# Performance work log

Hardware: AMD Instinct MI355X
Metric: run time of the kernel (lower is better)

The kernel has to match this reference:

```python
import jax, jax.numpy as jnp
import numpy as np

E = 200_000   # edges (messages)
T = 2_000_000 # triplets
N = 20_000    # atoms/nodes
H = 128       # hidden_channels
INT = 64      # int_emb_size
BAS = 8       # basis_emb_size
OUT_EMB = 256 # out_emb_channels
NRAD = 6
SBF_DIM = 7 * 6  # num_spherical * num_radial = 42
NB = 4        # num_blocks
OUTC = 1      # num_targets


def setup_inputs() -> dict:
    key = jax.random.key(0)
    ks = iter(jax.random.split(key, 64))

    def w(shape):
        # glorot-ish scaled weights, stored as [in, out] for x @ W
        return jax.random.normal(next(ks), shape, jnp.float32) / np.sqrt(shape[-2])

    return dict(
        x=jax.random.normal(next(ks), (E, H), jnp.float32),
        rbf=jax.random.normal(next(ks), (E, NRAD), jnp.float32),
        sbf=jax.random.normal(next(ks), (T, SBF_DIM), jnp.float32),
        # interaction block params, stacked over NB blocks
        W_rbf1=w((NB, NRAD, BAS)), W_rbf2=w((NB, BAS, H)),
        W_sbf1=w((NB, SBF_DIM, BAS)), W_sbf2=w((NB, BAS, INT)),
        W_kj=w((NB, H, H)), b_kj=jnp.zeros((NB, H), jnp.float32),
        W_ji=w((NB, H, H)), b_ji=jnp.zeros((NB, H), jnp.float32),
        W_down=w((NB, H, INT)), W_up=w((NB, INT, H)),
        Wb=w((NB, 2, H, H)), bb=jnp.zeros((NB, 2, H), jnp.float32),   # num_before_skip=1 -> 2 linears
        Wa=w((NB, 4, H, H)), ba=jnp.zeros((NB, 4, H), jnp.float32),   # num_after_skip=2 -> 4 linears
        W_lin=w((NB, H, H)), b_lin=jnp.zeros((NB, H), jnp.float32),
        # output block params, stacked over NB+1 blocks
        Wo_rbf=w((NB + 1, NRAD, H)),
        Wo_up=w((NB + 1, H, OUT_EMB)), bo_up=jnp.zeros((NB + 1, OUT_EMB), jnp.float32),
        Wo_lins=w((NB + 1, 3, OUT_EMB, OUT_EMB)), bo_lins=jnp.zeros((NB + 1, 3, OUT_EMB), jnp.float32),
        Wo_out=w((NB + 1, OUT_EMB, OUTC)),
        idx_kj=jax.random.randint(next(ks), (T,), 0, E, jnp.int32),
        idx_ji=jax.random.randint(next(ks), (T,), 0, E, jnp.int32),
        idx_i=jax.random.randint(next(ks), (E,), 0, N, jnp.int32),
        num_nodes=N,
    )


def _interaction(b, x, rbf, sbf, idx_kj, idx_ji, p):
    act = jax.nn.silu
    x_ji = act(x @ p['W_ji'][b] + p['b_ji'][b])
    x_kj = act(x @ p['W_kj'][b] + p['b_kj'][b])
    rbf_t = (rbf @ p['W_rbf1'][b]) @ p['W_rbf2'][b]          # [E,H]
    x_kj = act((x_kj * rbf_t) @ p['W_down'][b])              # [E,INT]
    sbf_t = (sbf @ p['W_sbf1'][b]) @ p['W_sbf2'][b]          # [T,INT]
    m = x_kj[idx_kj] * sbf_t                                  # triplet gather [T,INT]
    agg = jax.ops.segment_sum(m, idx_ji, num_segments=x.shape[0])  # scatter-add [E,INT]
    x_kj = act(agg @ p['W_up'][b])                            # [E,H]
    h = x_ji + x_kj
    # residual layers before skip (1 layer = 2 linears)
    h = h + act(act(h @ p['Wb'][b, 0] + p['bb'][b, 0]) @ p['Wb'][b, 1] + p['bb'][b, 1])
    h = act(h @ p['W_lin'][b] + p['b_lin'][b]) + x
    # residual layers after skip (2 layers = 4 linears)
    for l in range(2):
        h = h + act(act(h @ p['Wa'][b, 2 * l] + p['ba'][b, 2 * l]) @ p['Wa'][b, 2 * l + 1] + p['ba'][b, 2 * l + 1])
    return h


def _output(b, x, rbf, idx_i, num_nodes, p):
    act = jax.nn.silu
    t = (rbf @ p['Wo_rbf'][b]) * x                            # [E,H]
    t = jax.ops.segment_sum(t, idx_i, num_segments=num_nodes) # [N,H]
    t = t @ p['Wo_up'][b] + p['bo_up'][b]
    for l in range(3):
        t = act(t @ p['Wo_lins'][b, l] + p['bo_lins'][b, l])
    return t @ p['Wo_out'][b]                                 # [N,OUTC]


def reference(x, rbf, sbf, W_rbf1, W_rbf2, W_sbf1, W_sbf2, W_kj, b_kj, W_ji, b_ji,
              W_down, W_up, Wb, bb, Wa, ba, W_lin, b_lin,
              Wo_rbf, Wo_up, bo_up, Wo_lins, bo_lins, Wo_out,
              idx_kj, idx_ji, idx_i, num_nodes):
    p = dict(W_rbf1=W_rbf1, W_rbf2=W_rbf2, W_sbf1=W_sbf1, W_sbf2=W_sbf2,
             W_kj=W_kj, b_kj=b_kj, W_ji=W_ji, b_ji=b_ji, W_down=W_down, W_up=W_up,
             Wb=Wb, bb=bb, Wa=Wa, ba=ba, W_lin=W_lin, b_lin=b_lin,
             Wo_rbf=Wo_rbf, Wo_up=Wo_up, bo_up=bo_up,
             Wo_lins=Wo_lins, bo_lins=bo_lins, Wo_out=Wo_out)
    P = _output(0, x, rbf, idx_i, num_nodes, p)
    for b in range(NB):  # fixed small layer loop
        x = _interaction(b, x, rbf, sbf, idx_kj, idx_ji, p)
        P = P + _output(b + 1, x, rbf, idx_i, num_nodes, p)
    return P
```

## Files before the change

kernel.cpp:

```cpp
#include <hip/hip_runtime.h>
#include <hip/hip_bf16.h>

#define E_EDGES 200000
#define T_TRIP  2000000
#define N_NODES 20000
#define H_DIM   128
#define INT_DIM 64
#define BAS     8
#define OUT_EMB 256
#define NRAD    6
#define SBF_D   42
#define NB      4

typedef __attribute__((ext_vector_type(8))) __bf16 bf16x8;
typedef __attribute__((ext_vector_type(4))) float f32x4;
typedef unsigned short u16;

__device__ __forceinline__ float silu_f(float v) { return v / (1.0f + __expf(-v)); }

__device__ __forceinline__ u16 f2bf(float f) {
    unsigned int u = __float_as_uint(f);
    u += 0x7FFF + ((u >> 16) & 1);
    return (u16)(u >> 16);
}
__device__ __forceinline__ float bf2f(u16 h) {
    return __uint_as_float(((unsigned int)h) << 16);
}

__device__ __forceinline__ void st_split4(char* H, char* L, int row, int col0, int stride,
                                          const float v[4]) {
    ushort4 hh, ll;
    u16 h0 = f2bf(v[0]); ll.x = f2bf(v[0] - bf2f(h0)); hh.x = h0;
    u16 h1 = f2bf(v[1]); ll.y = f2bf(v[1] - bf2f(h1)); hh.y = h1;
    u16 h2 = f2bf(v[2]); ll.z = f2bf(v[2] - bf2f(h2)); hh.z = h2;
    u16 h3 = f2bf(v[3]); ll.w = f2bf(v[3] - bf2f(h3)); hh.w = h3;
    int off = (row * stride + col0 * 2) ^ ((row & 7) << 4);
    *reinterpret_cast<ushort4*>(H + off) = hh;
    *reinterpret_cast<ushort4*>(L + off) = ll;
}
__device__ __forceinline__ void ld_split4(const char* H, const char* L, int row, int col0,
                                          int stride, float v[4]) {
    int off = (row * stride + col0 * 2) ^ ((row & 7) << 4);
    ushort4 hh = *reinterpret_cast<const ushort4*>(H + off);
    ushort4 ll = *reinterpret_cast<const ushort4*>(L + off);
    v[0] = bf2f(hh.x) + bf2f(ll.x);
    v[1] = bf2f(hh.y) + bf2f(ll.y);
    v[2] = bf2f(hh.z) + bf2f(ll.z);
    v[3] = bf2f(hh.w) + bf2f(ll.w);
}
__device__ __forceinline__ void st_bf4(char* T, int row, int col0, int stride,
                                       const float v[4]) {
    ushort4 hh;
    hh.x = f2bf(v[0]); hh.y = f2bf(v[1]); hh.z = f2bf(v[2]); hh.w = f2bf(v[3]);
    int off = (row * stride + col0 * 2) ^ ((row & 7) << 4);
    *reinterpret_cast<ushort4*>(T + off) = hh;
}

struct BF8x4 { bf16x8 h[4]; bf16x8 l[4]; };

__device__ __forceinline__ BF8x4 loadB128f(const u16* __restrict__ Bh, const u16* __restrict__ Bl,
                                           int k0, int wn, int l15, int khalf)
{
    BF8x4 f;
    #pragma unroll
    for (int n = 0; n < 4; ++n) {
        size_t bo = (size_t)(wn * 64 + n * 16 + l15) * 128 + k0 + khalf;
        f.h[n] = *reinterpret_cast<const bf16x8*>(Bh + bo);
        f.l[n] = *reinterpret_cast<const bf16x8*>(Bl + bo);
    }
    return f;
}
__device__ __forceinline__ BF8x4 loadB64f(const u16* __restrict__ Bh, const u16* __restrict__ Bl,
                                          int k0, int wn, int l15, int khalf)
{
    BF8x4 f;
    #pragma unroll
    for (int n = 0; n < 4; ++n) {
        size_t bo = (size_t)(wn * 64 + n * 16 + l15) * 64 + k0 + khalf;
        f.h[n] = *reinterpret_cast<const bf16x8*>(Bh + bo);
        f.l[n] = *reinterpret_cast<const bf16x8*>(Bl + bo);
    }
    return f;
}
__device__ __forceinline__ BF8x4 loadB256f(const u16* __restrict__ Bh, const u16* __restrict__ Bl,
                                           int k0, int wn, int l15, int khalf)
{
    BF8x4 f;
    #pragma unroll
    for (int n = 0; n < 4; ++n) {
        size_t bo = (size_t)(wn * 64 + n * 16 + l15) * 256 + k0 + khalf;
        f.h[n] = *reinterpret_cast<const bf16x8*>(Bh + bo);
        f.l[n] = *reinterpret_cast<const bf16x8*>(Bl + bo);
    }
    return f;
}

__device__ __forceinline__ void mfma_cluster(
    const char* AH, const char* AL, int k0, int wm, int l15, int khalf,
    const BF8x4& b, f32x4 acc[2][4])
{
    __builtin_amdgcn_s_setprio(1);
    #pragma unroll
    for (int m = 0; m < 2; ++m) {
        int row = wm * 32 + m * 16 + l15;
        int off = (row * 256 + (k0 + khalf) * 2) ^ ((row & 7) << 4);
        bf16x8 ah = *reinterpret_cast<const bf16x8*>(AH + off);
        bf16x8 al = *reinterpret_cast<const bf16x8*>(AL + off);
        #pragma unroll
        for (int n = 0; n < 4; ++n) {
            acc[m][n] = __builtin_amdgcn_mfma_f32_16x16x32_bf16(b.h[n], ah, acc[m][n], 0, 0, 0);
            acc[m][n] = __builtin_amdgcn_mfma_f32_16x16x32_bf16(b.h[n], al, acc[m][n], 0, 0, 0);
            acc[m][n] = __builtin_amdgcn_mfma_f32_16x16x32_bf16(b.l[n], ah, acc[m][n], 0, 0, 0);
        }
    }
    __builtin_amdgcn_s_setprio(0);
}
__device__ __forceinline__ void mfma_cluster_T(
    const char* T, int k0, int wm, int l15, int khalf,
    const BF8x4& b, f32x4 acc[2][4])
{
    __builtin_amdgcn_s_setprio(1);
    #pragma unroll
    for (int m = 0; m < 2; ++m) {
        int row = wm * 32 + m * 16 + l15;
        int off = (row * 256 + (k0 + khalf) * 2) ^ ((row & 7) << 4);
        bf16x8 a = *reinterpret_cast<const bf16x8*>(T + off);
        #pragma unroll
        for (int n = 0; n < 4; ++n) {
            acc[m][n] = __builtin_amdgcn_mfma_f32_16x16x32_bf16(b.h[n], a, acc[m][n], 0, 0, 0);
            acc[m][n] = __builtin_amdgcn_mfma_f32_16x16x32_bf16(b.l[n], a, acc[m][n], 0, 0, 0);
        }
    }
    __builtin_amdgcn_s_setprio(0);
}
__device__ __forceinline__ void mfma_cluster64(
    const char* AH, const char* AL, int k0, int wm, int l15, int khalf,
    const BF8x4& b, f32x4 acc[2][4])
{
    __builtin_amdgcn_s_setprio(1);
    #pragma unroll
    for (int m = 0; m < 2; ++m) {
        int row = wm * 32 + m * 16 + l15;
        int off = (row * 128 + (k0 + khalf) * 2) ^ ((row & 7) << 4);
        bf16x8 ah = *reinterpret_cast<const bf16x8*>(AH + off);
        bf16x8 al = *reinterpret_cast<const bf16x8*>(AL + off);
        #pragma unroll
        for (int n = 0; n < 4; ++n) {
            acc[m][n] = __builtin_amdgcn_mfma_f32_16x16x32_bf16(b.h[n], ah, acc[m][n], 0, 0, 0);
            acc[m][n] = __builtin_amdgcn_mfma_f32_16x16x32_bf16(b.h[n], al, acc[m][n], 0, 0, 0);
            acc[m][n] = __builtin_amdgcn_mfma_f32_16x16x32_bf16(b.l[n], ah, acc[m][n], 0, 0, 0);
        }
    }
    __builtin_amdgcn_s_setprio(0);
}
__device__ __forceinline__ void mfma_cluster512(
    const char* AH, const char* AL, int k0, int l15, int khalf,
    const BF8x4& b, f32x4 acc[2][4])
{
    __builtin_amdgcn_s_setprio(1);
    #pragma unroll
    for (int m = 0; m < 2; ++m) {
        int row = m * 16 + l15;
        int off = (row * 512 + (k0 + khalf) * 2) ^ ((row & 7) << 4);
        bf16x8 ah = *reinterpret_cast<const bf16x8*>(AH + off);
        bf16x8 al = *reinterpret_cast<const bf16x8*>(AL + off);
        #pragma unroll
        for (int n = 0; n < 4; ++n) {
            acc[m][n] = __builtin_amdgcn_mfma_f32_16x16x32_bf16(b.h[n], ah, acc[m][n], 0, 0, 0);
            acc[m][n] = __builtin_amdgcn_mfma_f32_16x16x32_bf16(b.h[n], al, acc[m][n], 0, 0, 0);
            acc[m][n] = __builtin_amdgcn_mfma_f32_16x16x32_bf16(b.l[n], ah, acc[m][n], 0, 0, 0);
        }
    }
    __builtin_amdgcn_s_setprio(0);
}
__device__ __forceinline__ void mfma_cluster512_T(
    const char* T, int k0, int l15, int khalf,
    const BF8x4& b, f32x4 acc[2][4])
{
    __builtin_amdgcn_s_setprio(1);
    #pragma unroll
    for (int m = 0; m < 2; ++m) {
        int row = m * 16 + l15;
        int off = (row * 512 + (k0 + khalf) * 2) ^ ((row & 7) << 4);
        bf16x8 a = *reinterpret_cast<const bf16x8*>(T + off);
        #pragma unroll
        for (int n = 0; n < 4; ++n) {
            acc[m][n] = __builtin_amdgcn_mfma_f32_16x16x32_bf16(b.h[n], a, acc[m][n], 0, 0, 0);
            acc[m][n] = __builtin_amdgcn_mfma_f32_16x16x32_bf16(b.l[n], a, acc[m][n], 0, 0, 0);
        }
    }
    __builtin_amdgcn_s_setprio(0);
}

__device__ __forceinline__ void mm128_pipe(
    const char* AH, const char* AL,
    const u16* __restrict__ Bh, const u16* __restrict__ Bl, BF8x4& pre,
    const u16* __restrict__ nBh, const u16* __restrict__ nBl,
    int wm, int wn, int l15, int khalf, f32x4 acc[2][4])
{
    BF8x4 c0 = pre;
    BF8x4 c1 = loadB128f(Bh, Bl, 32, wn, l15, khalf);
    mfma_cluster(AH, AL, 0, wm, l15, khalf, c0, acc);
    BF8x4 c2 = loadB128f(Bh, Bl, 64, wn, l15, khalf);
    mfma_cluster(AH, AL, 32, wm, l15, khalf, c1, acc);
    BF8x4 c3 = loadB128f(Bh, Bl, 96, wn, l15, khalf);
    mfma_cluster(AH, AL, 64, wm, l15, khalf, c2, acc);
    if (nBh) pre = loadB128f(nBh, nBl, 0, wn, l15, khalf);
    mfma_cluster(AH, AL, 96, wm, l15, khalf, c3, acc);
}
__device__ __forceinline__ void mm128_pipe_T(
    const char* T,
    const u16* __restrict__ Bh, const u16* __restrict__ Bl, BF8x4& pre,
    const u16* __restrict__ nBh, const u16* __restrict__ nBl,
    int wm, int wn, int l15, int khalf, f32x4 acc[2][4])
{
    BF8x4 c0 = pre;
    BF8x4 c1 = loadB128f(Bh, Bl, 32, wn, l15, khalf);
    mfma_cluster_T(T, 0, wm, l15, khalf, c0, acc);
    BF8x4 c2 = loadB128f(Bh, Bl, 64, wn, l15, khalf);
    mfma_cluster_T(T, 32, wm, l15, khalf, c1, acc);
    BF8x4 c3 = loadB128f(Bh, Bl, 96, wn, l15, khalf);
    mfma_cluster_T(T, 64, wm, l15, khalf, c2, acc);
    if (nBh) pre = loadB128f(nBh, nBl, 0, wn, l15, khalf);
    mfma_cluster_T(T, 96, wm, l15, khalf, c3, acc);
}
__device__ __forceinline__ void mm64_pipe(
    const char* AH, const char* AL,
    const u16* __restrict__ Bh, const u16* __restrict__ Bl, BF8x4& pre,
    const u16* __restrict__ nBh, const u16* __restrict__ nBl,
    int wm, int wn, int l15, int khalf, f32x4 acc[2][4])
{
    BF8x4 c0 = pre;
    BF8x4 c1 = loadB64f(Bh, Bl, 32, wn, l15, khalf);
    mfma_cluster64(AH, AL, 0, wm, l15, khalf, c0, acc);
    if (nBh) pre = loadB128f(nBh, nBl, 0, wn, l15, khalf);
    mfma_cluster64(AH, AL, 32, wm, l15, khalf, c1, acc);
}

__global__ __launch_bounds__(256) void wprep(
    const float* __restrict__ src, u16* __restrict__ hi,
    u16* __restrict__ lo, int K, int N)
{
    int e = blockIdx.x * 256 + threadIdx.x;
    int total = K * N;
    if (e >= total) return;
    size_t base = (size_t)blockIdx.y * total;
    float a = src[base + e];
    int k = e / N, n = e - k * N;
    u16 h = f2bf(a);
    u16 l = f2bf(a - bf2f(h));
    hi[base + (size_t)n * K + k] = h;
    lo[base + (size_t)n * K + k] = l;
}

__global__ __launch_bounds__(256, 2) void pre_fuse(
    const float* __restrict__ X, const float* __restrict__ rbf,
    const float* __restrict__ W1,
    const u16* __restrict__ Wjih, const u16* __restrict__ Wjil, const float* __restrict__ bji,
    const u16* __restrict__ Wkjh, const u16* __restrict__ Wkjl, const float* __restrict__ bkj,
    const float* __restrict__ Wr2,
    const u16* __restrict__ Wdnh, const u16* __restrict__ Wdnl,
    float* __restrict__ E1, float* __restrict__ C1)
{
    __shared__ char smem[49152];
    char* XH = smem;
    char* XL = smem + 16384;
    char* IT = smem + 32768;

    const int tid  = threadIdx.x;
    const int lane = tid & 63;
    const int w    = tid >> 6;
    const int wm   = w >> 1, wn = w & 1;
    const int bm   = blockIdx.x * 64;
    const int l15  = lane & 15;
    const int khalf = (lane >> 4) * 8;
    const int r4   = (lane >> 4) * 4;

    BF8x4 pre = loadB128f(Wjih, Wjil, 0, wn, l15, khalf);

    {
        int r  = tid >> 2;
        int c0 = (tid & 3) * 32;
        const float* p = &X[(size_t)(bm + r) * H_DIM + c0];
        const int swz = (r & 7) << 4;
        #pragma unroll
        for (int q = 0; q < 8; ++q) {
            float4 f = *reinterpret_cast<const float4*>(p + q * 4);
            float vv[4] = {f.x, f.y, f.z, f.w};
            u16 h[4], l[4];
            #pragma unroll
            for (int j = 0; j < 4; ++j) {
                h[j] = f2bf(vv[j]);
                l[j] = f2bf(vv[j] - bf2f(h[j]));
            }
            int off = (r * 256 + c0 * 2 + q * 8) ^ swz;
            *reinterpret_cast<ushort4*>(XH + off) = make_ushort4(h[0], h[1], h[2], h[3]);
            *reinterpret_cast<ushort4*>(XL + off) = make_ushort4(l[0], l[1], l[2], l[3]);
        }
    }
    __syncthreads();

    {
        f32x4 acc[2][4] = {};
        mm128_pipe(XH, XL, Wjih, Wjil, pre, Wkjh, Wkjl, wm, wn, l15, khalf, acc);
        #pragma unroll
        for (int n = 0; n < 4; ++n) {
            int col0 = wn * 64 + n * 16 + r4;
            float4 bv = *reinterpret_cast<const float4*>(&bji[col0]);
            #pragma unroll
            for (int m = 0; m < 2; ++m) {
                int row = wm * 32 + m * 16 + l15;
                float4 o;
                o.x = silu_f(acc[m][n][0] + bv.x);
                o.y = silu_f(acc[m][n][1] + bv.y);
                o.z = silu_f(acc[m][n][2] + bv.z);
                o.w = silu_f(acc[m][n][3] + bv.w);
                *reinterpret_cast<float4*>(&E1[(size_t)(bm + row) * H_DIM + col0]) = o;
            }
        }
    }
    {
        f32x4 acc[2][4] = {};
        mm128_pipe(XH, XL, Wkjh, Wkjl, pre, nullptr, nullptr, wm, wn, l15, khalf, acc);
        float r8v[2][8];
        #pragma unroll
        for (int m = 0; m < 2; ++m) {
            int grow = bm + wm * 32 + m * 16 + l15;
            const float2* rp = reinterpret_cast<const float2*>(&rbf[(size_t)grow * NRAD]);
            float2 q0 = rp[0], q1 = rp[1], q2 = rp[2];
            float rv[NRAD] = {q0.x, q0.y, q1.x, q1.y, q2.x, q2.y};
            #pragma unroll
            for (int j = 0; j < 8; ++j) r8v[m][j] = 0.f;
            #pragma unroll
            for (int k = 0; k < NRAD; ++k)
                #pragma unroll
                for (int j = 0; j < 8; ++j)
                    r8v[m][j] = fmaf(rv[k], W1[k * BAS + j], r8v[m][j]);
        }
        #pragma unroll
        for (int n = 0; n < 4; ++n) {
            int col0 = wn * 64 + n * 16 + r4;
            float4 bvf = *reinterpret_cast<const float4*>(&bkj[col0]);
            float bv[4] = {bvf.x, bvf.y, bvf.z, bvf.w};
            float wrv[8][4];
            #pragma unroll
            for (int j = 0; j < 8; ++j) {
                float4 wf = *reinterpret_cast<const float4*>(&Wr2[j * H_DIM + col0]);
                wrv[j][0] = wf.x; wrv[j][1] = wf.y; wrv[j][2] = wf.z; wrv[j][3] = wf.w;
            }
            #pragma unroll
            for (int m = 0; m < 2; ++m) {
                int row = wm * 32 + m * 16 + l15;
                float v[4];
                #pragma unroll
                for (int r = 0; r < 4; ++r) {
                    float t = silu_f(acc[m][n][r] + bv[r]);
                    float g = 0.f;
                    #pragma unroll
                    for (int j = 0; j < 8; ++j)
                        g = fmaf(r8v[m][j], wrv[j][r], g);
                    v[r] = t * g;
                }
                st_bf4(IT, row, col0, 256, v);
            }
        }
    }
    __syncthreads();

    {
        f32x4 acc[2][2] = {};
        #pragma unroll
        for (int k0 = 0; k0 < 128; k0 += 32) {
            bf16x8 bh[2], bl[2];
            #pragma unroll
            for (int n = 0; n < 2; ++n) {
                size_t bo = (size_t)(wn * 32 + n * 16 + l15) * 128 + k0 + khalf;
                bh[n] = *reinterpret_cast<const bf16x8*>(Wdnh + bo);
                bl[n] = *reinterpret_cast<const bf16x8*>(Wdnl + bo);
            }
            __builtin_amdgcn_s_setprio(1);
            #pragma unroll
            for (int m = 0; m < 2; ++m) {
                int row = wm * 32 + m * 16 + l15;
                int off = (row * 256 + (k0 + khalf) * 2) ^ ((row & 7) << 4);
                bf16x8 a = *reinterpret_cast<const bf16x8*>(IT + off);
                #pragma unroll
                for (int n = 0; n < 2; ++n) {
                    acc[m][n] = __builtin_amdgcn_mfma_f32_16x16x32_bf16(bh[n], a, acc[m][n], 0, 0, 0);
                    acc[m][n] = __builtin_amdgcn_mfma_f32_16x16x32_bf16(bl[n], a, acc[m][n], 0, 0, 0);
                }
            }
            __builtin_amdgcn_s_setprio(0);
        }
        #pragma unroll
        for (int n = 0; n < 2; ++n) {
            int col0 = wn * 32 + n * 16 + r4;
            #pragma unroll
            for (int m = 0; m < 2; ++m) {
                int row = wm * 32 + m * 16 + l15;
                float4 o;
                o.x = silu_f(acc[m][n][0]);
                o.y = silu_f(acc[m][n][1]);
                o.z = silu_f(acc[m][n][2]);
                o.w = silu_f(acc[m][n][3]);
                *reinterpret_cast<float4*>(&C1[(size_t)(bm + row) * INT_DIM + col0]) = o;
            }
        }
    }
}

struct ChainP {
    const u16 *uph, *upl;
    const u16 *b0h, *b0l, *b1h, *b1l;
    const u16 *lnh, *lnl;
    const u16 *a0h, *a0l, *a1h, *a1l, *a2h, *a2l, *a3h, *a3l;
    const float *bb0, *bb1, *blin, *ba0, *ba1, *ba2, *ba3;
};
struct OutP {
    const float* TN;
    const u16 *Uh, *Ul; const float* bu;
    const u16 *L0h, *L0l; const float* b0;
    const u16 *L1h, *L1l; const float* b1;
    const u16 *L2h, *L2l; const float* b2;
    const float* Wo; float* P;
};

__device__ __forceinline__ void post_chain_body(
    char* smem, int bx,
    const float* __restrict__ AGG, const float* __restrict__ E1,
    const float* __restrict__ X, const ChainP& p, float* __restrict__ OUT)
{
    char* SH  = smem;
    char* SL  = smem + 16384;
    char* TMP = smem + 32768;
    char* GH  = TMP;
    char* GL  = TMP + 8192;

    const int tid  = threadIdx.x;
    const int lane = tid & 63;
    const int w    = tid >> 6;
    const int wm   = w >> 1, wn = w & 1;
    const int bm   = bx * 64;
    const int l15  = lane & 15;
    const int khalf = (lane >> 4) * 8;
    const int r4   = (lane >> 4) * 4;

    BF8x4 pre = loadB64f(p.uph, p.upl, 0, wn, l15, khalf);

    {
        int r  = tid >> 2;
        int c0 = (tid & 3) * 16;
        const float* pg = &AGG[(size_t)(bm + r) * INT_DIM + c0];
        const int swz = (r & 7) << 4;
        #pragma unroll
        for (int q = 0; q < 4; ++q) {
            float4 f = *reinterpret_cast<const float4*>(pg + q * 4);
            float vv[4] = {f.x, f.y, f.z, f.w};
            u16 h[4], l[4];
            #pragma unroll
            for (int j = 0; j < 4; ++j) {
                h[j] = f2bf(vv[j]);
                l[j] = f2bf(vv[j] - bf2f(h[j]));
            }
            int off = (r * 128 + c0 * 2 + q * 8) ^ swz;
            *reinterpret_cast<ushort4*>(GH + off) = make_ushort4(h[0], h[1], h[2], h[3]);
            *reinterpret_cast<ushort4*>(GL + off) = make_ushort4(l[0], l[1], l[2], l[3]);
        }
    }
    __syncthreads();

    f32x4 acc[2][4];
    #define ZACC { _Pragma("unroll") for (int m = 0; m < 2; ++m) \
                   _Pragma("unroll") for (int n = 0; n < 4; ++n) \
                       acc[m][n] = f32x4{0.f, 0.f, 0.f, 0.f}; }

    ZACC
    mm64_pipe(GH, GL, p.uph, p.upl, pre, p.b0h, p.b0l, wm, wn, l15, khalf, acc);
    #pragma unroll
    for (int n = 0; n < 4; ++n) {
        int col0 = wn * 64 + n * 16 + r4;
        #pragma unroll
        for (int m = 0; m < 2; ++m) {
            int row = wm * 32 + m * 16 + l15;
            float4 e = *reinterpret_cast<const float4*>(&E1[(size_t)(bm + row) * H_DIM + col0]);
            float v[4];
            v[0] = e.x + silu_f(acc[m][n][0]);
            v[1] = e.y + silu_f(acc[m][n][1]);
            v[2] = e.z + silu_f(acc[m][n][2]);
            v[3] = e.w + silu_f(acc[m][n][3]);
            st_split4(SH, SL, row, col0, 256, v);
        }
    }
    __syncthreads();

    #define STAGE_PLAIN(WH, WL, BIAS, NWH, NWL)                                         \
    {                                                                                   \
        ZACC                                                                            \
        mm128_pipe(SH, SL, WH, WL, pre, NWH, NWL, wm, wn, l15, khalf, acc);             \
        _Pragma("unroll")                                                               \
        for (int n = 0; n < 4; ++n) {                                                   \
            int col0 = wn * 64 + n * 16 + r4;                                           \
            float4 bv = *reinterpret_cast<const float4*>(&BIAS[col0]);                  \
            _Pragma("unroll")                                                           \
            for (int m = 0; m < 2; ++m) {                                               \
                int row = wm * 32 + m * 16 + l15;                                       \
                float v[4];                                                             \
                v[0] = silu_f(acc[m][n][0] + bv.x);                                     \
                v[1] = silu_f(acc[m][n][1] + bv.y);                                     \
                v[2] = silu_f(acc[m][n][2] + bv.z);                                     \
                v[3] = silu_f(acc[m][n][3] + bv.w);                                     \
                st_bf4(TMP, row, col0, 256, v);                                         \
            }                                                                           \
        }                                                                               \
        __syncthreads();                                                                \
    }

    #define STAGE_RES(WH, WL, BIAS, NWH, NWL)                                           \
    {                                                                                   \
        ZACC                                                                            \
        mm128_pipe_T(TMP, WH, WL, pre, NWH, NWL, wm, wn, l15, khalf, acc);              \
        _Pragma("unroll")                                                               \
        for (int n = 0; n < 4; ++n) {                                                   \
            int col0 = wn * 64 + n * 16 + r4;                                           \
            float4 bv = *reinterpret_cast<const float4*>(&BIAS[col0]);                  \
            _Pragma("unroll")                                                           \
            for (int m = 0; m < 2; ++m) {                                               \
                int row = wm * 32 + m * 16 + l15;                                       \
                float v[4];                                                             \
                ld_split4(SH, SL, row, col0, 256, v);                                   \
                v[0] += silu_f(acc[m][n][0] + bv.x);                                    \
                v[1] += silu_f(acc[m][n][1] + bv.y);                                    \
                v[2] += silu_f(acc[m][n][2] + bv.z);                                    \
                v[3] += silu_f(acc[m][n][3] + bv.w);                                    \
                st_split4(SH, SL, row, col0, 256, v);                                   \
            }                                                                           \
        }                                                                               \
        __syncthreads();                                                                \
    }

    STAGE_PLAIN(p.b0h, p.b0l, p.bb0, p.b1h, p.b1l)
    STAGE_RES(p.b1h, p.b1l, p.bb1, p.lnh, p.lnl)

    {
        ZACC
        mm128_pipe(SH, SL, p.lnh, p.lnl, pre, p.a0h, p.a0l, wm, wn, l15, khalf, acc);
        __syncthreads();
        #pragma unroll
        for (int n = 0; n < 4; ++n) {
            int col0 = wn * 64 + n * 16 + r4;
            float4 bv = *reinterpret_cast<const float4*>(&p.blin[col0]);
            #pragma unroll
            for (int m = 0; m < 2; ++m) {
                int row = wm * 32 + m * 16 + l15;
                float4 xv = *reinterpret_cast<const float4*>(&X[(size_t)(bm + row) * H_DIM + col0]);
                float v[4];
                v[0] = silu_f(acc[m][n][0] + bv.x) + xv.x;
                v[1] = silu_f(acc[m][n][1] + bv.y) + xv.y;
                v[2] = silu_f(acc[m][n][2] + bv.z) + xv.z;
                v[3] = silu_f(acc[m][n][3] + bv.w) + xv.w;
                st_split4(SH, SL, row, col0, 256, v);
            }
        }
        __syncthreads();
    }

    STAGE_PLAIN(p.a0h, p.a0l, p.ba0, p.a1h, p.a1l)
    STAGE_RES(p.a1h, p.a1l, p.ba1, p.a2h, p.a2l)
    STAGE_PLAIN(p.a2h, p.a2l, p.ba2, p.a3h, p.a3l)

    {
        ZACC
        mm128_pipe_T(TMP, p.a3h, p.a3l, pre, nullptr, nullptr, wm, wn, l15, khalf, acc);
        #pragma unroll
        for (int n = 0; n < 4; ++n) {
            int col0 = wn * 64 + n * 16 + r4;
            float4 bv = *reinterpret_cast<const float4*>(&p.ba3[col0]);
            #pragma unroll
            for (int m = 0; m < 2; ++m) {
                int row = wm * 32 + m * 16 + l15;
                float v[4];
                ld_split4(SH, SL, row, col0, 256, v);
                float4 o;
                o.x = v[0] + silu_f(acc[m][n][0] + bv.x);
                o.y = v[1] + silu_f(acc[m][n][1] + bv.y);
                o.z = v[2] + silu_f(acc[m][n][2] + bv.z);
                o.w = v[3] + silu_f(acc[m][n][3] + bv.w);
                *reinterpret_cast<float4*>(&OUT[(size_t)(bm + row) * H_DIM + col0]) = o;
            }
        }
    }
    #undef STAGE_PLAIN
    #undef STAGE_RES
    #undef ZACC
}

__device__ __forceinline__ void out_chain_body(char* smem, int bx, const OutP& o)
{
    char* SH  = smem;
    char* SL  = smem + 16384;
    char* TMP = smem + 32768;
    char* XH  = TMP;
    char* XL  = TMP + 8192;

    const int tid  = threadIdx.x;
    const int lane = tid & 63;
    const int wn   = tid >> 6;
    const int bm   = bx * 32;
    const int l15  = lane & 15;
    const int khalf = (lane >> 4) * 8;
    const int r4   = (lane >> 4) * 4;

    {
        int r  = tid >> 3;
        int c0 = (tid & 7) * 16;
        const float* p = &o.TN[(size_t)(bm + r) * H_DIM + c0];
        const int swz = (r & 7) << 4;
        #pragma unroll
        for (int q = 0; q < 4; ++q) {
            float4 f = *reinterpret_cast<const float4*>(p + q * 4);
            float vv[4] = {f.x, f.y, f.z, f.w};
            u16 h[4], l[4];
            #pragma unroll
            for (int j = 0; j < 4; ++j) {
                h[j] = f2bf(vv[j]);
                l[j] = f2bf(vv[j] - bf2f(h[j]));
            }
            int off = (r * 256 + c0 * 2 + q * 8) ^ swz;
            *reinterpret_cast<ushort4*>(XH + off) = make_ushort4(h[0], h[1], h[2], h[3]);
            *reinterpret_cast<ushort4*>(XL + off) = make_ushort4(l[0], l[1], l[2], l[3]);
        }
    }
    __syncthreads();

    f32x4 acc[2][4];
    #define ZACC { _Pragma("unroll") for (int m = 0; m < 2; ++m) \
                   _Pragma("unroll") for (int n = 0; n < 4; ++n) \
                       acc[m][n] = f32x4{0.f, 0.f, 0.f, 0.f}; }

    {
        ZACC
        BF8x4 cur = loadB128f(o.Uh, o.Ul, 0, wn, l15, khalf);
        #pragma unroll
        for (int k = 0; k < 4; ++k) {
            BF8x4 nxt;
            if (k < 3) nxt = loadB128f(o.Uh, o.Ul, 32 * (k + 1), wn, l15, khalf);
            mfma_cluster(XH, XL, 32 * k, 0, l15, khalf, cur, acc);
            if (k < 3) cur = nxt;
        }
        __syncthreads();
        #pragma unroll
        for (int n = 0; n < 4; ++n) {
            int col0 = wn * 64 + n * 16 + r4;
            float4 bv = *reinterpret_cast<const float4*>(&o.bu[col0]);
            #pragma unroll
            for (int m = 0; m < 2; ++m) {
                int row = m * 16 + l15;
                float v[4] = {acc[m][n][0] + bv.x, acc[m][n][1] + bv.y,
                              acc[m][n][2] + bv.z, acc[m][n][3] + bv.w};
                st_split4(SH, SL, row, col0, 512, v);
            }
        }
        __syncthreads();
    }

    {
        ZACC
        BF8x4 cur = loadB256f(o.L0h, o.L0l, 0, wn, l15, khalf);
        #pragma unroll
        for (int k = 0; k < 8; ++k) {
            BF8x4 nxt;
            if (k < 7) nxt = loadB256f(o.L0h, o.L0l, 32 * (k + 1), wn, l15, khalf);
            mfma_cluster512(SH, SL, 32 * k, l15, khalf, cur, acc);
            if (k < 7) cur = nxt;
        }
        #pragma unroll
        for (int n = 0; n < 4; ++n) {
            int col0 = wn * 64 + n * 16 + r4;
            float4 bv = *reinterpret_cast<const float4*>(&o.b0[col0]);
            #pragma unroll
            for (int m = 0; m < 2; ++m) {
                int row = m * 16 + l15;
                float v[4];
                v[0] = silu_f(acc[m][n][0] + bv.x);
                v[1] = silu_f(acc[m][n][1] + bv.y);
                v[2] = silu_f(acc[m][n][2] + bv.z);
                v[3] = silu_f(acc[m][n][3] + bv.w);
                st_bf4(TMP, row, col0, 512, v);
            }
        }
        __syncthreads();
    }

    {
        ZACC
        BF8x4 cur = loadB256f(o.L1h, o.L1l, 0, wn, l15, khalf);
        #pragma unroll
        for (int k = 0; k < 8; ++k) {
            BF8x4 nxt;
            if (k < 7) nxt = loadB256f(o.L1h, o.L1l, 32 * (k + 1), wn, l15, khalf);
            mfma_cluster512_T(TMP, 32 * k, l15, khalf, cur, acc);
            if (k < 7) cur = nxt;
        }
        #pragma unroll
        for (int n = 0; n < 4; ++n) {
            int col0 = wn * 64 + n * 16 + r4;
            float4 bv = *reinterpret_cast<const float4*>(&o.b1[col0]);
            #pragma unroll
            for (int m = 0; m < 2; ++m) {
                int row = m * 16 + l15;
                float v[4];
                v[0] = silu_f(acc[m][n][0] + bv.x);
                v[1] = silu_f(acc[m][n][1] + bv.y);
                v[2] = silu_f(acc[m][n][2] + bv.z);
                v[3] = silu_f(acc[m][n][3] + bv.w);
                st_split4(SH, SL, row, col0, 512, v);
            }
        }
        __syncthreads();
    }

    {
        ZACC
        BF8x4 cur = loadB256f(o.L2h, o.L2l, 0, wn, l15, khalf);
        #pragma unroll
        for (int k = 0; k < 8; ++k) {
            BF8x4 nxt;
            if (k < 7) nxt = loadB256f(o.L2h, o.L2l, 32 * (k + 1), wn, l15, khalf);
            mfma_cluster512(SH, SL, 32 * k, l15, khalf, cur, acc);
            if (k < 7) cur = nxt;
        }
        __syncthreads();
        #pragma unroll
        for (int n = 0; n < 4; ++n) {
            int col0 = wn * 64 + n * 16 + r4;
            float4 bv = *reinterpret_cast<const float4*>(&o.b2[col0]);
            #pragma unroll
            for (int m = 0; m < 2; ++m) {
                int row = m * 16 + l15;
                float v[4];
                v[0] = silu_f(acc[m][n][0] + bv.x);
                v[1] = silu_f(acc[m][n][1] + bv.y);
                v[2] = silu_f(acc[m][n][2] + bv.z);
                v[3] = silu_f(acc[m][n][3] + bv.w);
                st_split4(SH, SL, row, col0, 512, v);
            }
        }
// ... 417 lines not shown
```

Baseline: 4.103 ms.

## Give each wave full-width row strips in edge MLP chains and drop block barriers

```diff
diff --git a/kernel.cpp b/kernel.cpp
--- a/kernel.cpp
+++ b/kernel.cpp
@@ -56,6 +56,79 @@
     *reinterpret_cast<ushort4*>(T + off) = hh;
 }
 
+template<int NT>
+__device__ __forceinline__ void wave_mm128s(
+    const char* AH, const char* AL, int rb,
+    const u16* __restrict__ Bh, const u16* __restrict__ Bl,
+    int l15, int khalf, f32x4 acc[NT])
+{
+    const int row = rb + l15;
+    #pragma unroll
+    for (int k0 = 0; k0 < 128; k0 += 32) {
+        int off = (row * 256 + (k0 + khalf) * 2) ^ ((row & 7) << 4);
+        bf16x8 ah = *reinterpret_cast<const bf16x8*>(AH + off);
+        bf16x8 al = *reinterpret_cast<const bf16x8*>(AL + off);
+        __builtin_amdgcn_s_setprio(1);
+        #pragma unroll
+        for (int n = 0; n < NT; ++n) {
+            size_t bo = (size_t)(n * 16 + l15) * 128 + k0 + khalf;
+            bf16x8 bh = *reinterpret_cast<const bf16x8*>(Bh + bo);
+            bf16x8 bl = *reinterpret_cast<const bf16x8*>(Bl + bo);
+            acc[n] = __builtin_amdgcn_mfma_f32_16x16x32_bf16(bh, ah, acc[n], 0, 0, 0);
+            acc[n] = __builtin_amdgcn_mfma_f32_16x16x32_bf16(bh, al, acc[n], 0, 0, 0);
+            acc[n] = __builtin_amdgcn_mfma_f32_16x16x32_bf16(bl, ah, acc[n], 0, 0, 0);
+        }
+        __builtin_amdgcn_s_setprio(0);
+    }
+}
+template<int NT>
+__device__ __forceinline__ void wave_mm128t(
+    const char* T, int rb,
+    const u16* __restrict__ Bh, const u16* __restrict__ Bl,
+    int l15, int khalf, f32x4 acc[NT])
+{
+    const int row = rb + l15;
+    #pragma unroll
+    for (int k0 = 0; k0 < 128; k0 += 32) {
+        int off = (row * 256 + (k0 + khalf) * 2) ^ ((row & 7) << 4);
+        bf16x8 a = *reinterpret_cast<const bf16x8*>(T + off);
+        __builtin_amdgcn_s_setprio(1);
+        #pragma unroll
+        for (int n = 0; n < NT; ++n) {
+            size_t bo = (size_t)(n * 16 + l15) * 128 + k0 + khalf;
+            bf16x8 bh = *reinterpret_cast<const bf16x8*>(Bh + bo);
+            bf16x8 bl = *reinterpret_cast<const bf16x8*>(Bl + bo);
+            acc[n] = __builtin_amdgcn_mfma_f32_16x16x32_bf16(bh, a, acc[n], 0, 0, 0);
+            acc[n] = __builtin_amdgcn_mfma_f32_16x16x32_bf16(bl, a, acc[n], 0, 0, 0);
+        }
+        __builtin_amdgcn_s_setprio(0);
+    }
+}
+__device__ __forceinline__ void wave_mm64s(
+    const char* AH, const char* AL, int rb,
+    const u16* __restrict__ Bh, const u16* __restrict__ Bl,
+    int l15, int khalf, f32x4 acc[8])
+{
+    const int row = rb + l15;
+    #pragma unroll
+    for (int k0 = 0; k0 < 64; k0 += 32) {
+        int off = (row * 128 + (k0 + khalf) * 2) ^ ((row & 7) << 4);
+        bf16x8 ah = *reinterpret_cast<const bf16x8*>(AH + off);
+        bf16x8 al = *reinterpret_cast<const bf16x8*>(AL + off);
+        __builtin_amdgcn_s_setprio(1);
+        #pragma unroll
+        for (int n = 0; n < 8; ++n) {
+            size_t bo = (size_t)(n * 16 + l15) * 64 + k0 + khalf;
+            bf16x8 bh = *reinterpret_cast<const bf16x8*>(Bh + bo);
+            bf16x8 bl = *reinterpret_cast<const bf16x8*>(Bl + bo);
+            acc[n] = __builtin_amdgcn_mfma_f32_16x16x32_bf16(bh, ah, acc[n], 0, 0, 0);
+            acc[n] = __builtin_amdgcn_mfma_f32_16x16x32_bf16(bh, al, acc[n], 0, 0, 0);
+            acc[n] = __builtin_amdgcn_mfma_f32_16x16x32_bf16(bl, ah, acc[n], 0, 0, 0);
+        }
+        __builtin_amdgcn_s_setprio(0);
+    }
+}
+
 struct BF8x4 { bf16x8 h[4]; bf16x8 l[4]; };
 
 __device__ __forceinline__ BF8x4 loadB128f(const u16* __restrict__ Bh, const u16* __restrict__ Bl,
@@ -70,18 +143,6 @@
     }
     return f;
 }
-__device__ __forceinline__ BF8x4 loadB64f(const u16* __restrict__ Bh, const u16* __restrict__ Bl,
-                                          int k0, int wn, int l15, int khalf)
-{
-    BF8x4 f;
-    #pragma unroll
-    for (int n = 0; n < 4; ++n) {
-        size_t bo = (size_t)(wn * 64 + n * 16 + l15) * 64 + k0 + khalf;
-        f.h[n] = *reinterpret_cast<const bf16x8*>(Bh + bo);
-        f.l[n] = *reinterpret_cast<const bf16x8*>(Bl + bo);
-    }
-    return f;
-}
 __device__ __forceinline__ BF8x4 loadB256f(const u16* __restrict__ Bh, const u16* __restrict__ Bl,
                                            int k0, int wn, int l15, int khalf)
 {
@@ -94,7 +155,6 @@
     }
     return f;
 }
-
 __device__ __forceinline__ void mfma_cluster(
     const char* AH, const char* AL, int k0, int wm, int l15, int khalf,
     const BF8x4& b, f32x4 acc[2][4])
@@ -115,44 +175,6 @@
     }
     __builtin_amdgcn_s_setprio(0);
 }
-__device__ __forceinline__ void mfma_cluster_T(
-    const char* T, int k0, int wm, int l15, int khalf,
-    const BF8x4& b, f32x4 acc[2][4])
-{
-    __builtin_amdgcn_s_setprio(1);
-    #pragma unroll
-    for (int m = 0; m < 2; ++m) {
-        int row = wm * 32 + m * 16 + l15;
-        int off = (row * 256 + (k0 + khalf) * 2) ^ ((row & 7) << 4);
-        bf16x8 a = *reinterpret_cast<const bf16x8*>(T + off);
-        #pragma unroll
-        for (int n = 0; n < 4; ++n) {
-            acc[m][n] = __builtin_amdgcn_mfma_f32_16x16x32_bf16(b.h[n], a, acc[m][n], 0, 0, 0);
-            acc[m][n] = __builtin_amdgcn_mfma_f32_16x16x32_bf16(b.l[n], a, acc[m][n], 0, 0, 0);
-        }
-    }
-    __builtin_amdgcn_s_setprio(0);
-}
-__device__ __forceinline__ void mfma_cluster64(
-    const char* AH, const char* AL, int k0, int wm, int l15, int khalf,
-    const BF8x4& b, f32x4 acc[2][4])
-{
-    __builtin_amdgcn_s_setprio(1);
-    #pragma unroll
-    for (int m = 0; m < 2; ++m) {
-        int row = wm * 32 + m * 16 + l15;
-        int off = (row * 128 + (k0 + khalf) * 2) ^ ((row & 7) << 4);
-        bf16x8 ah = *reinterpret_cast<const bf16x8*>(AH + off);
-        bf16x8 al = *reinterpret_cast<const bf16x8*>(AL + off);
-        #pragma unroll
-        for (int n = 0; n < 4; ++n) {
-            acc[m][n] = __builtin_amdgcn_mfma_f32_16x16x32_bf16(b.h[n], ah, acc[m][n], 0, 0, 0);
-            acc[m][n] = __builtin_amdgcn_mfma_f32_16x16x32_bf16(b.h[n], al, acc[m][n], 0, 0, 0);
-            acc[m][n] = __builtin_amdgcn_mfma_f32_16x16x32_bf16(b.l[n], ah, acc[m][n], 0, 0, 0);
-        }
-    }
-    __builtin_amdgcn_s_setprio(0);
-}
 __device__ __forceinline__ void mfma_cluster512(
     const char* AH, const char* AL, int k0, int l15, int khalf,
     const BF8x4& b, f32x4 acc[2][4])
@@ -190,51 +212,6 @@
         }
     }
     __builtin_amdgcn_s_setprio(0);
-}
-
-__device__ __forceinline__ void mm128_pipe(
-    const char* AH, const char* AL,
-    const u16* __restrict__ Bh, const u16* __restrict__ Bl, BF8x4& pre,
-    const u16* __restrict__ nBh, const u16* __restrict__ nBl,
-    int wm, int wn, int l15, int khalf, f32x4 acc[2][4])
-{
-    BF8x4 c0 = pre;
-    BF8x4 c1 = loadB128f(Bh, Bl, 32, wn, l15, khalf);
-    mfma_cluster(AH, AL, 0, wm, l15, khalf, c0, acc);
-    BF8x4 c2 = loadB128f(Bh, Bl, 64, wn, l15, khalf);
-    mfma_cluster(AH, AL, 32, wm, l15, khalf, c1, acc);
-    BF8x4 c3 = loadB128f(Bh, Bl, 96, wn, l15, khalf);
-    mfma_cluster(AH, AL, 64, wm, l15, khalf, c2, acc);
-    if (nBh) pre = loadB128f(nBh, nBl, 0, wn, l15, khalf);
-    mfma_cluster(AH, AL, 96, wm, l15, khalf, c3, acc);
-}
-__device__ __forceinline__ void mm128_pipe_T(
-    const char* T,
-    const u16* __restrict__ Bh, const u16* __restrict__ Bl, BF8x4& pre,
-    const u16* __restrict__ nBh, const u16* __restrict__ nBl,
-    int wm, int wn, int l15, int khalf, f32x4 acc[2][4])
-{
-    BF8x4 c0 = pre;
-    BF8x4 c1 = loadB128f(Bh, Bl, 32, wn, l15, khalf);
-    mfma_cluster_T(T, 0, wm, l15, khalf, c0, acc);
-    BF8x4 c2 = loadB128f(Bh, Bl, 64, wn, l15, khalf);
-    mfma_cluster_T(T, 32, wm, l15, khalf, c1, acc);
-    BF8x4 c3 = loadB128f(Bh, Bl, 96, wn, l15, khalf);
-    mfma_cluster_T(T, 64, wm, l15, khalf, c2, acc);
-    if (nBh) pre = loadB128f(nBh, nBl, 0, wn, l15, khalf);
-    mfma_cluster_T(T, 96, wm, l15, khalf, c3, acc);
-}
-__device__ __forceinline__ void mm64_pipe(
-    const char* AH, const char* AL,
-    const u16* __restrict__ Bh, const u16* __restrict__ Bl, BF8x4& pre,
-    const u16* __restrict__ nBh, const u16* __restrict__ nBl,
-    int wm, int wn, int l15, int khalf, f32x4 acc[2][4])
-{
-    BF8x4 c0 = pre;
-    BF8x4 c1 = loadB64f(Bh, Bl, 32, wn, l15, khalf);
-    mfma_cluster64(AH, AL, 0, wm, l15, khalf, c0, acc);
-    if (nBh) pre = loadB128f(nBh, nBl, 0, wn, l15, khalf);
-    mfma_cluster64(AH, AL, 32, wm, l15, khalf, c1, acc);
 }
 
 __global__ __launch_bounds__(256) void wprep(
@@ -270,13 +247,12 @@
     const int tid  = threadIdx.x;
     const int lane = tid & 63;
     const int w    = tid >> 6;
-    const int wm   = w >> 1, wn = w & 1;
+    const int rb   = w * 16;
     const int bm   = blockIdx.x * 64;
     const int l15  = lane & 15;
     const int khalf = (lane >> 4) * 8;
     const int r4   = (lane >> 4) * 4;
-
-    BF8x4 pre = loadB128f(Wjih, Wjil, 0, wn, l15, khalf);
+    const int row  = rb + l15;
 
     {
         int r  = tid >> 2;
@@ -298,113 +274,68 @@
             *reinterpret_cast<ushort4*>(XL + off) = make_ushort4(l[0], l[1], l[2], l[3]);
         }
     }
-    __syncthreads();
-
-    {
-        f32x4 acc[2][4] = {};
-        mm128_pipe(XH, XL, Wjih, Wjil, pre, Wkjh, Wkjl, wm, wn, l15, khalf, acc);
-        #pragma unroll
-        for (int n = 0; n < 4; ++n) {
-            int col0 = wn * 64 + n * 16 + r4;
+
+    {
+        f32x4 acc[8] = {};
+        wave_mm128s<8>(XH, XL, rb, Wjih, Wjil, l15, khalf, acc);
+        #pragma unroll
+        for (int n = 0; n < 8; ++n) {
+            int col0 = n * 16 + r4;
             float4 bv = *reinterpret_cast<const float4*>(&bji[col0]);
-            #pragma unroll
-            for (int m = 0; m < 2; ++m) {
-                int row = wm * 32 + m * 16 + l15;
-                float4 o;
-                o.x = silu_f(acc[m][n][0] + bv.x);
-                o.y = silu_f(acc[m][n][1] + bv.y);
-                o.z = silu_f(acc[m][n][2] + bv.z);
-                o.w = silu_f(acc[m][n][3] + bv.w);
-                *reinterpret_cast<float4*>(&E1[(size_t)(bm + row) * H_DIM + col0]) = o;
-            }
-        }
-    }
-    {
-        f32x4 acc[2][4] = {};
-        mm128_pipe(XH, XL, Wkjh, Wkjl, pre, nullptr, nullptr, wm, wn, l15, khalf, acc);
-        float r8v[2][8];
-        #pragma unroll
-        for (int m = 0; m < 2; ++m) {
-            int grow = bm + wm * 32 + m * 16 + l15;
-            const float2* rp = reinterpret_cast<const float2*>(&rbf[(size_t)grow * NRAD]);
+            float4 o;
+            o.x = silu_f(acc[n][0] + bv.x);
+            o.y = silu_f(acc[n][1] + bv.y);
+            o.z = silu_f(acc[n][2] + bv.z);
+            o.w = silu_f(acc[n][3] + bv.w);
+            *reinterpret_cast<float4*>(&E1[(size_t)(bm + row) * H_DIM + col0]) = o;
+        }
+    }
+    {
+        f32x4 acc[8] = {};
+        wave_mm128s<8>(XH, XL, rb, Wkjh, Wkjl, l15, khalf, acc);
+        float r8v[8];
+        {
+            const float2* rp = reinterpret_cast<const float2*>(&rbf[(size_t)(bm + row) * NRAD]);
             float2 q0 = rp[0], q1 = rp[1], q2 = rp[2];
             float rv[NRAD] = {q0.x, q0.y, q1.x, q1.y, q2.x, q2.y};
             #pragma unroll
-            for (int j = 0; j < 8; ++j) r8v[m][j] = 0.f;
+            for (int j = 0; j < 8; ++j) r8v[j] = 0.f;
             #pragma unroll
             for (int k = 0; k < NRAD; ++k)
                 #pragma unroll
                 for (int j = 0; j < 8; ++j)
-                    r8v[m][j] = fmaf(rv[k], W1[k * BAS + j], r8v[m][j]);
-        }
-        #pragma unroll
-        for (int n = 0; n < 4; ++n) {
-            int col0 = wn * 64 + n * 16 + r4;
+                    r8v[j] = fmaf(rv[k], W1[k * BAS + j], r8v[j]);
+        }
+        #pragma unroll
+        for (int n = 0; n < 8; ++n) {
+            int col0 = n * 16 + r4;
             float4 bvf = *reinterpret_cast<const float4*>(&bkj[col0]);
             float bv[4] = {bvf.x, bvf.y, bvf.z, bvf.w};
-            float wrv[8][4];
+            float v[4];
             #pragma unroll
-            for (int j = 0; j < 8; ++j) {
-                float4 wf = *reinterpret_cast<const float4*>(&Wr2[j * H_DIM + col0]);
-                wrv[j][0] = wf.x; wrv[j][1] = wf.y; wrv[j][2] = wf.z; wrv[j][3] = wf.w;
+            for (int r = 0; r < 4; ++r) {
+                float t = silu_f(acc[n][r] + bv[r]);
+                float g = 0.f;
+                #pragma unroll
+                for (int j = 0; j < 8; ++j)
+                    g = fmaf(r8v[j], Wr2[j * H_DIM + col0 + r], g);
+                v[r] = t * g;
             }
-            #pragma unroll
-            for (int m = 0; m < 2; ++m) {
-                int row = wm * 32 + m * 16 + l15;
-                float v[4];
-                #pragma unroll
-                for (int r = 0; r < 4; ++r) {
-                    float t = silu_f(acc[m][n][r] + bv[r]);
-                    float g = 0.f;
-                    #pragma unroll
-                    for (int j = 0; j < 8; ++j)
-                        g = fmaf(r8v[m][j], wrv[j][r], g);
-                    v[r] = t * g;
-                }
-                st_bf4(IT, row, col0, 256, v);
-            }
-        }
-    }
-    __syncthreads();
-
-    {
-        f32x4 acc[2][2] = {};
-        #pragma unroll
-        for (int k0 = 0; k0 < 128; k0 += 32) {
-            bf16x8 bh[2], bl[2];
-            #pragma unroll
-            for (int n = 0; n < 2; ++n) {
-                size_t bo = (size_t)(wn * 32 + n * 16 + l15) * 128 + k0 + khalf;
-                bh[n] = *reinterpret_cast<const bf16x8*>(Wdnh + bo);
-                bl[n] = *reinterpret_cast<const bf16x8*>(Wdnl + bo);
-            }
-            __builtin_amdgcn_s_setprio(1);
-            #pragma unroll
-            for (int m = 0; m < 2; ++m) {
-                int row = wm * 32 + m * 16 + l15;
-                int off = (row * 256 + (k0 + khalf) * 2) ^ ((row & 7) << 4);
-                bf16x8 a = *reinterpret_cast<const bf16x8*>(IT + off);
-                #pragma unroll
-                for (int n = 0; n < 2; ++n) {
-                    acc[m][n] = __builtin_amdgcn_mfma_f32_16x16x32_bf16(bh[n], a, acc[m][n], 0, 0, 0);
-                    acc[m][n] = __builtin_amdgcn_mfma_f32_16x16x32_bf16(bl[n], a, acc[m][n], 0, 0, 0);
-                }
-            }
-            __builtin_amdgcn_s_setprio(0);
-        }
-        #pragma unroll
-        for (int n = 0; n < 2; ++n) {
-            int col0 = wn * 32 + n * 16 + r4;
-            #pragma unroll
-            for (int m = 0; m < 2; ++m) {
-                int row = wm * 32 + m * 16 + l15;
-                float4 o;
-                o.x = silu_f(acc[m][n][0]);
-                o.y = silu_f(acc[m][n][1]);
-                o.z = silu_f(acc[m][n][2]);
-                o.w = silu_f(acc[m][n][3]);
-                *reinterpret_cast<float4*>(&C1[(size_t)(bm + row) * INT_DIM + col0]) = o;
-            }
+            st_bf4(IT, row, col0, 256, v);
+        }
+    }
+    {
+        f32x4 acc[4] = {};
+        wave_mm128t<4>(IT, rb, Wdnh, Wdnl, l15, khalf, acc);
+        #pragma unroll
+        for (int n = 0; n < 4; ++n) {
+            int col0 = n * 16 + r4;
+            float4 o;
+            o.x = silu_f(acc[n][0]);
+            o.y = silu_f(acc[n][1]);
+            o.z = silu_f(acc[n][2]);
+            o.w = silu_f(acc[n][3]);
+            *reinterpret_cast<float4*>(&C1[(size_t)(bm + row) * INT_DIM + col0]) = o;
         }
     }
 }
@@ -439,13 +370,12 @@
     const int tid  = threadIdx.x;
     const int lane = tid & 63;
     const int w    = tid >> 6;
-    const int wm   = w >> 1, wn = w & 1;
+    const int rb   = w * 16;
     const int bm   = bx * 64;
     const int l15  = lane & 15;
     const int khalf = (lane >> 4) * 8;
     const int r4   = (lane >> 4) * 4;
-
-    BF8x4 pre = loadB64f(p.uph, p.upl, 0, wn, l15, khalf);
+    const int row  = rb + l15;
 
     {
         int r  = tid >> 2;
@@ -467,131 +397,104 @@
             *reinterpret_cast<ushort4*>(GL + off) = make_ushort4(l[0], l[1], l[2], l[3]);
         }
     }
-    __syncthreads();
-
-    f32x4 acc[2][4];
-    #define ZACC { _Pragma("unroll") for (int m = 0; m < 2; ++m) \
-                   _Pragma("unroll") for (int n = 0; n < 4; ++n) \
-                       acc[m][n] = f32x4{0.f, 0.f, 0.f, 0.f}; }
-
-    ZACC
-    mm64_pipe(GH, GL, p.uph, p.upl, pre, p.b0h, p.b0l, wm, wn, l15, khalf, acc);
-    #pragma unroll
-    for (int n = 0; n < 4; ++n) {
-        int col0 = wn * 64 + n * 16 + r4;
-        #pragma unroll
-        for (int m = 0; m < 2; ++m) {
-            int row = wm * 32 + m * 16 + l15;
-            float4 e = *reinterpret_cast<const float4*>(&E1[(size_t)(bm + row) * H_DIM + col0]);
+
+    f32x4 acc[8];
+    #define ZACC8 { _Pragma("unroll") for (int n = 0; n < 8; ++n) \
+                        acc[n] = f32x4{0.f, 0.f, 0.f, 0.f}; }
+
+    ZACC8
+    wave_mm64s(GH, GL, rb, p.uph, p.upl, l15, khalf, acc);
+    #pragma unroll
+    for (int n = 0; n < 8; ++n) {
+        int col0 = n * 16 + r4;
+        float4 e = *reinterpret_cast<const float4*>(&E1[(size_t)(bm + row) * H_DIM + col0]);
+        float v[4];
+        v[0] = e.x + silu_f(acc[n][0]);
+        v[1] = e.y + silu_f(acc[n][1]);
+        v[2] = e.z + silu_f(acc[n][2]);
+        v[3] = e.w + silu_f(acc[n][3]);
+        st_split4(SH, SL, row, col0, 256, v);
+    }
+
+    #define STAGE_PLAIN(WH, WL, BIAS)                                                   \
+    {                                                                                   \
+        ZACC8                                                                           \
+        wave_mm128s<8>(SH, SL, rb, WH, WL, l15, khalf, acc);                            \
+        _Pragma("unroll")                                                               \
+        for (int n = 0; n < 8; ++n) {                                                   \
+            int col0 = n * 16 + r4;                                                     \
+            float4 bv = *reinterpret_cast<const float4*>(&BIAS[col0]);                  \
+            float v[4];                                                                 \
+            v[0] = silu_f(acc[n][0] + bv.x);                                            \
+            v[1] = silu_f(acc[n][1] + bv.y);                                            \
+            v[2] = silu_f(acc[n][2] + bv.z);                                            \
+            v[3] = silu_f(acc[n][3] + bv.w);                                            \
+            st_bf4(TMP, row, col0, 256, v);                                             \
+        }                                                                               \
+    }
+
+    #define STAGE_RES(WH, WL, BIAS)                                                     \
+    {                                                                                   \
+        ZACC8                                                                           \
+        wave_mm128t<8>(TMP, rb, WH, WL, l15, khalf, acc);                               \
+        _Pragma("unroll")                                                               \
+        for (int n = 0; n < 8; ++n) {                                                   \
+            int col0 = n * 16 + r4;                                                     \
+            float4 bv = *reinterpret_cast<const float4*>(&BIAS[col0]);                  \
+            float v[4];                                                                 \
+            ld_split4(SH, SL, row, col0, 256, v);                                       \
+            v[0] += silu_f(acc[n][0] + bv.x);                                           \
+            v[1] += silu_f(acc[n][1] + bv.y);                                           \
+            v[2] += silu_f(acc[n][2] + bv.z);                                           \
+            v[3] += silu_f(acc[n][3] + bv.w);                                           \
+            st_split4(SH, SL, row, col0, 256, v);                                       \
+        }                                                                               \
+    }
+
+    STAGE_PLAIN(p.b0h, p.b0l, p.bb0)
+    STAGE_RES(p.b1h, p.b1l, p.bb1)
+
+    {
+        ZACC8
+        wave_mm128s<8>(SH, SL, rb, p.lnh, p.lnl, l15, khalf, acc);
+        #pragma unroll
+        for (int n = 0; n < 8; ++n) {
+            int col0 = n * 16 + r4;
+            float4 bv = *reinterpret_cast<const float4*>(&p.blin[col0]);
+            float4 xv = *reinterpret_cast<const float4*>(&X[(size_t)(bm + row) * H_DIM + col0]);
             float v[4];
-            v[0] = e.x + silu_f(acc[m][n][0]);
-            v[1] = e.y + silu_f(acc[m][n][1]);
-            v[2] = e.z + silu_f(acc[m][n][2]);
-            v[3] = e.w + silu_f(acc[m][n][3]);
+            v[0] = silu_f(acc[n][0] + bv.x) + xv.x;
+            v[1] = silu_f(acc[n][1] + bv.y) + xv.y;
+            v[2] = silu_f(acc[n][2] + bv.z) + xv.z;
+            v[3] = silu_f(acc[n][3] + bv.w) + xv.w;
             st_split4(SH, SL, row, col0, 256, v);
         }
     }
-    __syncthreads();
-
-    #define STAGE_PLAIN(WH, WL, BIAS, NWH, NWL)                                         \
-    {                                                                                   \
-        ZACC                                                                            \
-        mm128_pipe(SH, SL, WH, WL, pre, NWH, NWL, wm, wn, l15, khalf, acc);             \
-        _Pragma("unroll")                                                               \
-        for (int n = 0; n < 4; ++n) {                                                   \
-            int col0 = wn * 64 + n * 16 + r4;                                           \
-            float4 bv = *reinterpret_cast<const float4*>(&BIAS[col0]);                  \
-            _Pragma("unroll")                                                           \
-            for (int m = 0; m < 2; ++m) {                                               \
-                int row = wm * 32 + m * 16 + l15;                                       \
-                float v[4];                                                             \
-                v[0] = silu_f(acc[m][n][0] + bv.x);                                     \
-                v[1] = silu_f(acc[m][n][1] + bv.y);                                     \
-                v[2] = silu_f(acc[m][n][2] + bv.z);                                     \
-                v[3] = silu_f(acc[m][n][3] + bv.w);                                     \
-                st_bf4(TMP, row, col0, 256, v);                                         \
-            }                                                                           \
-        }                                                                               \
-        __syncthreads();                                                                \
-    }
-
-    #define STAGE_RES(WH, WL, BIAS, NWH, NWL)                                           \
-    {                                                                                   \
-        ZACC                                                                            \
-        mm128_pipe_T(TMP, WH, WL, pre, NWH, NWL, wm, wn, l15, khalf, acc);              \
-        _Pragma("unroll")                                                               \
-        for (int n = 0; n < 4; ++n) {                                                   \
-            int col0 = wn * 64 + n * 16 + r4;                                           \
-            float4 bv = *reinterpret_cast<const float4*>(&BIAS[col0]);                  \
-            _Pragma("unroll")                                                           \
-            for (int m = 0; m < 2; ++m) {                                               \
-                int row = wm * 32 + m * 16 + l15;                                       \
-                float v[4];                                                             \
-                ld_split4(SH, SL, row, col0, 256, v);                                   \
-                v[0] += silu_f(acc[m][n][0] + bv.x);                                    \
-                v[1] += silu_f(acc[m][n][1] + bv.y);                                    \
-                v[2] += silu_f(acc[m][n][2] + bv.z);                                    \
-                v[3] += silu_f(acc[m][n][3] + bv.w);                                    \
-                st_split4(SH, SL, row, col0, 256, v);                                   \
-            }                                                                           \
-        }                                                                               \
-        __syncthreads();                                                                \
-    }
-
-    STAGE_PLAIN(p.b0h, p.b0l, p.bb0, p.b1h, p.b1l)
-    STAGE_RES(p.b1h, p.b1l, p.bb1, p.lnh, p.lnl)
-
-    {
-        ZACC
-        mm128_pipe(SH, SL, p.lnh, p.lnl, pre, p.a0h, p.a0l, wm, wn, l15, khalf, acc);
-        __syncthreads();
-        #pragma unroll
-        for (int n = 0; n < 4; ++n) {
-            int col0 = wn * 64 + n * 16 + r4;
-            float4 bv = *reinterpret_cast<const float4*>(&p.blin[col0]);
-            #pragma unroll
-            for (int m = 0; m < 2; ++m) {
-                int row = wm * 32 + m * 16 + l15;
-                float4 xv = *reinterpret_cast<const float4*>(&X[(size_t)(bm + row) * H_DIM + col0]);
-                float v[4];
-                v[0] = silu_f(acc[m][n][0] + bv.x) + xv.x;
-                v[1] = silu_f(acc[m][n][1] + bv.y) + xv.y;
-                v[2] = silu_f(acc[m][n][2] + bv.z) + xv.z;
-                v[3] = silu_f(acc[m][n][3] + bv.w) + xv.w;
-                st_split4(SH, SL, row, col0, 256, v);
-            }
-        }
-        __syncthreads();
-    }
-
-    STAGE_PLAIN(p.a0h, p.a0l, p.ba0, p.a1h, p.a1l)
-    STAGE_RES(p.a1h, p.a1l, p.ba1, p.a2h, p.a2l)
-    STAGE_PLAIN(p.a2h, p.a2l, p.ba2, p.a3h, p.a3l)
-
-    {
-        ZACC
-        mm128_pipe_T(TMP, p.a3h, p.a3l, pre, nullptr, nullptr, wm, wn, l15, khalf, acc);
-        #pragma unroll
-        for (int n = 0; n < 4; ++n) {
-            int col0 = wn * 64 + n * 16 + r4;
+
+    STAGE_PLAIN(p.a0h, p.a0l, p.ba0)
+    STAGE_RES(p.a1h, p.a1l, p.ba1)
+    STAGE_PLAIN(p.a2h, p.a2l, p.ba2)
+
+    {
+        ZACC8
+        wave_mm128t<8>(TMP, rb, p.a3h, p.a3l, l15, khalf, acc);
+        #pragma unroll
+        for (int n = 0; n < 8; ++n) {
+            int col0 = n * 16 + r4;
             float4 bv = *reinterpret_cast<const float4*>(&p.ba3[col0]);
-            #pragma unroll
-            for (int m = 0; m < 2; ++m) {
-                int row = wm * 32 + m * 16 + l15;
-                float v[4];
-                ld_split4(SH, SL, row, col0, 256, v);
-                float4 o;
-                o.x = v[0] + silu_f(acc[m][n][0] + bv.x);
-                o.y = v[1] + silu_f(acc[m][n][1] + bv.y);
-                o.z = v[2] + silu_f(acc[m][n][2] + bv.z);
-                o.w = v[3] + silu_f(acc[m][n][3] + bv.w);
-                *reinterpret_cast<float4*>(&OUT[(size_t)(bm + row) * H_DIM + col0]) = o;
-            }
+            float v[4];
+            ld_split4(SH, SL, row, col0, 256, v);
+            float4 o;
+            o.x = v[0] + silu_f(acc[n][0] + bv.x);
+            o.y = v[1] + silu_f(acc[n][1] + bv.y);
+            o.z = v[2] + silu_f(acc[n][2] + bv.z);
+            o.w = v[3] + silu_f(acc[n][3] + bv.w);
+            *reinterpret_cast<float4*>(&OUT[(size_t)(bm + row) * H_DIM + col0]) = o;
         }
     }
     #undef STAGE_PLAIN
     #undef STAGE_RES
-    #undef ZACC
+    #undef ZACC8
 }
 
 __device__ __forceinline__ void out_chain_body(char* smem, int bx, const OutP& o)
```

New measurement: 5.698 ms. 1.39x slower.
